# Kernel tuning notes

Measured on AMD Instinct MI355X. Metric: run time of the kernel, lower is better.

Reference implementation:

```python
import jax, jax.numpy as jnp
import numpy as np

B, T, DIM, HEADS, KV_HEADS = 2, 2048, 1024, 16, 4
HD = DIM // HEADS  # 64


def _rope(t, sin, cos):
    # interleaved RoPE: pairs (2i, 2i+1) rotated by the same angle
    rot = jnp.stack([-t[..., 1::2], t[..., ::2]], axis=-1).reshape(t.shape)
    return t * cos + rot * sin


def setup_inputs() -> dict:
    key = jax.random.key(0)
    kx, kq, kk, kv, ko = jax.random.split(key, 5)
    x = jax.random.normal(kx, (B, T, DIM), dtype=jnp.float32)
    # standard RoPE tables, [T, HD]
    pos = jnp.arange(T, dtype=jnp.float32)
    inv_freq = 1.0 / (10000.0 ** (jnp.arange(0, HD, 2, dtype=jnp.float32) / HD))
    ang = pos[:, None] * inv_freq[None, :]  # [T, HD/2]
    sin = jnp.repeat(jnp.sin(ang), 2, axis=-1)  # [T, HD]
    cos = jnp.repeat(jnp.cos(ang), 2, axis=-1)
    mask = jnp.ones((B, 1, T), dtype=jnp.float32)  # padding mask (all valid)
    s = 1.0 / np.sqrt(DIM).astype(np.float32)
    Wq = jax.random.normal(kq, (DIM, DIM), dtype=jnp.float32) * s
    Wk = jax.random.normal(kk, (DIM, KV_HEADS * HD), dtype=jnp.float32) * s
    Wv = jax.random.normal(kv, (DIM, KV_HEADS * HD), dtype=jnp.float32) * s
    Wo = jax.random.normal(ko, (DIM, DIM), dtype=jnp.float32) * s
    return {"x": x, "sin": sin, "cos": cos, "mask": mask,
            "Wq": Wq, "Wk": Wk, "Wv": Wv, "Wo": Wo}


def reference(x, sin, cos, mask, Wq, Wk, Wv, Wo):
    Bx, Tx, C = x.shape
    # projections -> [B, H, T, HD] / [B, KV, T, HD]
    q = (x @ Wq).reshape(Bx, Tx, HEADS, HD).transpose(0, 2, 1, 3)
    k = (x @ Wk).reshape(Bx, Tx, KV_HEADS, HD).transpose(0, 2, 1, 3)
    v = (x @ Wv).reshape(Bx, Tx, KV_HEADS, HD).transpose(0, 2, 1, 3)
    # RoPE (sin/cos [T, HD] broadcast over batch/heads)
    q = _rope(q, sin, cos)
    k = _rope(k, sin, cos)
    # GQA: expand kv heads to query heads
    groups = HEADS // KV_HEADS
    k = jnp.repeat(k, groups, axis=1)
    v = jnp.repeat(v, groups, axis=1)
    scores = jnp.einsum('bhqd,bhkd->bhqk', q, k) / np.sqrt(HD).astype(np.float32)
    causal = jnp.tril(jnp.ones((Tx, Tx), dtype=bool))  # [T, T]
    m = (mask[:, None, :, :] > 0) & causal  # [B,1,1,T] & [T,T] -> [B,1,T,T]
    scores = jnp.where(m, scores, jnp.asarray(-1e9, scores.dtype))
    attn = jax.nn.softmax(scores, axis=-1)
    out = jnp.einsum('bhqk,bhkd->bhqd', attn, v)
    out = out.transpose(0, 2, 1, 3).reshape(Bx, Tx, C)
    return out @ Wo
```

## Files before the change

### kernel.cpp

```cpp
#include <hip/hip_runtime.h>
#include <math.h>

typedef __attribute__((ext_vector_type(8))) short bf16x8;
typedef __attribute__((ext_vector_type(4))) float f32x4;
typedef __attribute__((ext_vector_type(4))) unsigned short u16x4;

#define B_    2
#define T_    2048
#define DIM_  1024
#define H_    16
#define KV_   4
#define HD_   64

#define QSCALE 0.1803368801111437f
#define SOFF  24.0f

static __device__ __forceinline__ unsigned short f2bf(float f) {
    union { float f; unsigned int u; } v; v.f = f;
    unsigned int r = v.u + 0x7fff + ((v.u >> 16) & 1);
    return (unsigned short)(r >> 16);
}

static __device__ __forceinline__ unsigned int pkbf(float lo, float hi) {
    union { float f; unsigned int u; } a, b; a.f = lo; b.f = hi;
    return ((a.u + 0x8000u) >> 16) | ((b.u + 0x8000u) & 0xffff0000u);
}

static __device__ __forceinline__ void gload16(const void* g, void* l) {
    __builtin_amdgcn_global_load_lds(
        (const __attribute__((address_space(1))) unsigned int*)g,
        (__attribute__((address_space(3))) unsigned int*)l, 16, 0, 0);
}

#define MFMA16(a, b, c) __builtin_amdgcn_mfma_f32_16x16x32_bf16(a, b, c, 0, 0, 0)

#define XB_OFF   0u
#define WT_OFF   4194304u
#define WOT_OFF  5767168u
#define QB_OFF   6815744u
#define KB_OFF   11010048u
#define VTB_OFF  12058624u
#define AB_OFF   13107200u
#define MB_OFF   17301504u

static __device__ __forceinline__ void wtrans_body(
    const float* __restrict__ W, unsigned short* __restrict__ Wt, int N,
    int n0, int k0, int tid, float (*Ts)[65])
{
    const int r = tid >> 4, c4 = (tid & 15) * 4;
    #pragma unroll
    for (int i = 0; i < 4; ++i) {
        float4 v = *(const float4*)&W[(size_t)(k0 + r + 16 * i) * N + n0 + c4];
        Ts[r + 16 * i][c4 + 0] = v.x; Ts[r + 16 * i][c4 + 1] = v.y;
        Ts[r + 16 * i][c4 + 2] = v.z; Ts[r + 16 * i][c4 + 3] = v.w;
    }
    __syncthreads();
    const int rn = tid >> 3, ck = (tid & 7) * 8;
    #pragma unroll
    for (int i = 0; i < 2; ++i) {
        int n = rn + 32 * i;
        unsigned short u[8];
        #pragma unroll
        for (int e = 0; e < 8; ++e) u[e] = f2bf(Ts[ck + e][n]);
        *(bf16x8*)&Wt[(size_t)(n0 + n) * 1024 + k0 + ck] = *(bf16x8*)u;
    }
}

__global__ __launch_bounds__(256) void prepass_kernel(
    const float* __restrict__ x,
    const float* __restrict__ Wq, const float* __restrict__ Wk,
    const float* __restrict__ Wv, const float* __restrict__ Wo,
    const float* __restrict__ maskp,
    unsigned short* __restrict__ xb, unsigned short* __restrict__ Wt,
    unsigned short* __restrict__ Wot, float* __restrict__ mbias)
{
    __shared__ float Ts[64][65];
    const int blk = blockIdx.x, tid = threadIdx.x;

    if (blk < 2048) {
        const size_t i = ((size_t)blk * 256 + tid) * 8;
        float4 a = *(const float4*)&x[i];
        float4 b = *(const float4*)&x[i + 4];
        unsigned short u[8] = {f2bf(a.x), f2bf(a.y), f2bf(a.z), f2bf(a.w),
                               f2bf(b.x), f2bf(b.y), f2bf(b.z), f2bf(b.w)};
        *(bf16x8*)&xb[i] = *(bf16x8*)u;
    } else if (blk < 2304) {
        const int sb = blk - 2048;
        wtrans_body(Wq, Wt, 1024, (sb & 15) * 64, (sb >> 4) * 64, tid, Ts);
    } else if (blk < 2368) {
        const int sb = blk - 2304;
        wtrans_body(Wk, Wt + 1024u * 1024u, 256, (sb & 3) * 64, (sb >> 2) * 64,
                    tid, Ts);
    } else if (blk < 2432) {
        const int sb = blk - 2368;
        wtrans_body(Wv, Wt + 1280u * 1024u, 256, (sb & 3) * 64, (sb >> 2) * 64,
                    tid, Ts);
    } else if (blk < 2688) {
        const int sb = blk - 2432;
        wtrans_body(Wo, Wot, 1024, (sb & 15) * 64, (sb >> 4) * 64, tid, Ts);
    } else {
        #pragma unroll
        for (int e = 0; e < 4; ++e) {
            const int i = tid * 16 + e * 4;
            f32x4 mv = *(const f32x4*)&maskp[i];
            f32x4 bv;
            #pragma unroll
            for (int j = 0; j < 4; ++j) bv[j] = mv[j] > 0.f ? -SOFF : -1e30f;
            *(f32x4*)&mbias[i] = bv;
        }
    }
}

__global__ __launch_bounds__(256) void qkv_mfma_kernel(
    const unsigned short* __restrict__ xb, const unsigned short* __restrict__ Wt,
    const float* __restrict__ sinp, const float* __restrict__ cosp,
    unsigned short* __restrict__ Qw, unsigned short* __restrict__ Kw,
    unsigned short* __restrict__ Vtw)
{
    __shared__ __align__(16) unsigned char As[8192];
    __shared__ __align__(16) unsigned char Bs[16384];

    const int tid = threadIdx.x, lane = tid & 63, w = tid >> 6;
    const int lr = lane & 15, lg = lane >> 4;
    const int wm = w >> 1, wn = w & 1;
    const int bn = blockIdx.x, bm = blockIdx.y;
    const int m0 = bm * 64, n0 = bn * 128;

    const int chunkR = lane >> 3;
    const int srcOff = 8 * ((lane & 7) ^ chunkR);

    f32x4 acc[2][4] = {};

    for (int k0 = 0; k0 < 1024; k0 += 64) {
        __syncthreads();
        #pragma unroll
        for (int i = 0; i < 6; ++i) {
            const int c = w * 6 + i;
            if (c < 8) {
                const int row = c * 8 + chunkR;
                gload16(xb + (size_t)(m0 + row) * 1024 + k0 + srcOff, As + c * 1024);
            } else {
                const int row = (c - 8) * 8 + chunkR;
                gload16(Wt + (size_t)(n0 + row) * 1024 + k0 + srcOff,
                        Bs + (c - 8) * 1024);
            }
        }
        __syncthreads();
        #pragma unroll
        for (int kk = 0; kk < 2; ++kk) {
            bf16x8 af[2], bfr[4];
            #pragma unroll
            for (int mf = 0; mf < 2; ++mf) {
                const int row = wm * 32 + mf * 16 + lr;
                af[mf] = *(const bf16x8*)(As + row * 128 +
                          ((kk * 64 + lg * 16) ^ ((row & 7) << 4)));
            }
            #pragma unroll
            for (int nf = 0; nf < 4; ++nf) {
                const int row = wn * 64 + nf * 16 + lr;
                bfr[nf] = *(const bf16x8*)(Bs + row * 128 +
                          ((kk * 64 + lg * 16) ^ ((row & 7) << 4)));
            }
            #pragma unroll
            for (int mf = 0; mf < 2; ++mf)
                #pragma unroll
                for (int nf = 0; nf < 4; ++nf)
                    acc[mf][nf] = MFMA16(af[mf], bfr[nf], acc[mf][nf]);
        }
    }

    const float rsign = (lane & 1) ? 1.f : -1.f;
    #pragma unroll
    for (int nf = 0; nf < 4; ++nf) {
        const int col = n0 + wn * 64 + nf * 16 + lr;
        #pragma unroll
        for (int mf = 0; mf < 2; ++mf) {
            const int mrow = m0 + wm * 32 + mf * 16 + lg * 4;
            const int b = mrow >> 11;
            const int t0 = mrow & 2047;
            if (col < 1280) {
                const int d = col & 63;
                #pragma unroll
                for (int r = 0; r < 4; ++r) {
                    float val = acc[mf][nf][r];
                    float partner = __shfl_xor(val, 1);
                    const int t = t0 + r;
                    float cs = cosp[t * 64 + d], sn = sinp[t * 64 + d];
                    float rv = val * cs + rsign * partner * sn;
                    if (col < 1024) {
                        const int h = col >> 6;
                        Qw[(((size_t)b * H_ + h) * T_ + t) * 64 + d] =
                            f2bf(rv * QSCALE);
                    } else {
                        const int kv = (col - 1024) >> 6;
                        char* krow = (char*)Kw +
                            ((((size_t)b * KV_ + kv) * T_ + t) << 7);
                        *(unsigned short*)(krow + ((2 * d) ^ ((t & 7) << 4))) =
                            f2bf(rv);
                    }
                }
            } else {
                const int cv = col - 1280, kv = cv >> 6, d = cv & 63;
                unsigned short u[4];
                #pragma unroll
                for (int r = 0; r < 4; ++r) u[r] = f2bf(acc[mf][nf][r]);
                char* vrow = (char*)Vtw +
                    ((((size_t)b * KV_ + kv) * 64 + d) * (size_t)T_ * 2);
                *(u16x4*)(vrow + ((2 * t0) ^ ((d & 7) << 4))) = *(u16x4*)u;
            }
        }
    }
}

__global__ __launch_bounds__(512, 4) void attn_kernel(
    const unsigned short* __restrict__ Qg, const unsigned short* __restrict__ Kg,
    const unsigned short* __restrict__ Vtg, const float* __restrict__ mbias,
    unsigned short* __restrict__ attn_out)
{
    __shared__ __align__(16) unsigned char Kl[2][8192];
    __shared__ __align__(16) unsigned char Vl[2][8192];
    __shared__ __align__(16) unsigned char Pl[16384];
    __shared__ float Lb[256];

    const int tid  = threadIdx.x;
    const int lane = tid & 63;
    const int w    = tid >> 6;
    const int grp  = w >> 2;
    const int wq   = w & 3;
    const int lr   = lane & 15;
    const int lg   = lane >> 4;

    const int bi   = blockIdx.x;
    const int qt   = 31 - (bi >> 5);
    const int bh   = bi & 31;
    const int h    = bh & 15;
    const int b    = bh >> 4;
    const int kvh  = h >> 2;
    const int q0   = qt * 64;
    const int qrow = q0 + wq * 16 + lr;

    const int nt    = qt + 1;
    const int mid   = nt >> 1;
    const int iters = nt - mid;

    const char* Kb = (const char*)(Kg  + ((size_t)b * KV_ + kvh) * T_ * HD_);
    const char* Vb = (const char*)(Vtg + ((size_t)b * KV_ + kvh) * HD_ * T_);
    const float* brow = mbias + b * T_;

    const int sr  = lane >> 3;
    const int scb = (lane & 7) * 16;
    unsigned char* Pw = &Pl[w * 2048];

    const unsigned short* Qbase =
        Qg + (((size_t)b * H_ + h) * T_ + qrow) * HD_;
    const bf16x8 qf0 = *(const bf16x8*)(Qbase + lg * 8);
    const bf16x8 qf1 = *(const bf16x8*)(Qbase + 32 + lg * 8);

    f32x4 o[4] = {};
    float l = 0.f;

    for (int it = 0; it < iters; ++it) {
        const int ktg = grp ? (mid + it) : it;
        const bool active = grp || (it < mid);
        const int k0 = ktg * 64;

        if (active) {
            #pragma unroll
            for (int i = 0; i < 2; ++i) {
                const int rb  = wq * 2 + i;
                const int row = rb * 8 + sr;
                gload16(Kb + (size_t)(k0 + row) * 128 + scb, &Kl[grp][rb * 1024]);
                gload16(Vb + (size_t)row * 4096 + 2 * k0 + scb, &Vl[grp][rb * 1024]);
            }
        }
        __syncthreads();

        if (active) {
            const unsigned char* Kc = Kl[grp];
            const unsigned char* Vc = Vl[grp];

            f32x4 bv[4];
            #pragma unroll
            for (int n = 0; n < 4; ++n)
                bv[n] = *(const f32x4*)&brow[k0 + 16 * n + 4 * lg];

            f32x4 s[4] = {};
            __builtin_amdgcn_s_setprio(1);
            #pragma unroll
            for (int n = 0; n < 4; ++n) {
                const int key = 16 * n + lr;
                #pragma unroll
                for (int ks = 0; ks < 2; ++ks) {
                    bf16x8 kb = *(const bf16x8*)(Kc +
                        ((key * 128 + 64 * ks + lg * 16) ^ ((key & 7) << 4)));
                    s[n] = MFMA16(kb, ks == 0 ? qf0 : qf1, s[n]);
                }
            }
            __builtin_amdgcn_s_setprio(0);

            if (ktg == qt) {
                #pragma unroll
                for (int n = 0; n < 4; ++n)
                    #pragma unroll
                    for (int r = 0; r < 4; ++r) {
                        const int keyg = k0 + 16 * n + 4 * lg + r;
                        s[n][r] = (keyg <= qrow) ? s[n][r] + bv[n][r] : -1e30f;
                    }
            } else {
                #pragma unroll
                for (int n = 0; n < 4; ++n)
                    #pragma unroll
                    for (int r = 0; r < 4; ++r) s[n][r] += bv[n][r];
            }
            #pragma unroll
            for (int n = 0; n < 4; ++n)
                #pragma unroll
                for (int r = 0; r < 4; ++r)
                    s[n][r] = exp2f(s[n][r]);

            float tsum[4];
            #pragma unroll
            for (int n = 0; n < 4; ++n)
                tsum[n] = (s[n][0] + s[n][1]) + (s[n][2] + s[n][3]);
            l += (tsum[0] + tsum[1]) + (tsum[2] + tsum[3]);

            #pragma unroll
            for (int n = 0; n < 4; ++n) {
                uint2 wv;
                wv.x = pkbf(s[n][0], s[n][1]);
                wv.y = pkbf(s[n][2], s[n][3]);
                *(uint2*)(Pw + ((lr * 128 + 32 * n + 8 * lg) ^ ((lr & 7) << 4))) = wv;
            }
            bf16x8 pa0 = *(const bf16x8*)(Pw + ((lr * 128 +      lg * 16) ^ ((lr & 7) << 4)));
            bf16x8 pa1 = *(const bf16x8*)(Pw + ((lr * 128 + 64 + lg * 16) ^ ((lr & 7) << 4)));

            __builtin_amdgcn_s_setprio(1);
            #pragma unroll
            for (int n = 0; n < 4; ++n) {
                const int d = 16 * n + lr;
                #pragma unroll
                for (int ks = 0; ks < 2; ++ks) {
                    bf16x8 vb = *(const bf16x8*)(Vc +
                        ((d * 128 + 64 * ks + lg * 16) ^ ((d & 7) << 4)));
                    o[n] = MFMA16(vb, ks == 0 ? pa0 : pa1, o[n]);
                }
            }
            __builtin_amdgcn_s_setprio(0);
        }

        __syncthreads();
    }

    const int slot = wq * 64 + lane;
    if (grp) {
        float* ob = (float*)Pl;
        #pragma unroll
        for (int n = 0; n < 4; ++n)
            *(f32x4*)&ob[slot * 16 + n * 4] = o[n];
        Lb[slot] = l;
    }
    __syncthreads();
    if (!grp) {
        const float* ob = (const float*)Pl;
        #pragma unroll
        for (int n = 0; n < 4; ++n) {
            f32x4 obv = *(const f32x4*)&ob[slot * 16 + n * 4];
            o[n] += obv;
        }
        float lf = l + Lb[slot];
        lf += __shfl_xor(lf, 16);
        lf += __shfl_xor(lf, 32);
        const float linv = 1.f / lf;
        unsigned short* orow =
            attn_out + ((size_t)b * T_ + qrow) * DIM_ + h * HD_;
        #pragma unroll
        for (int n = 0; n < 4; ++n) {
            unsigned short u[4];
            #pragma unroll
            for (int r = 0; r < 4; ++r) u[r] = f2bf(o[n][r] * linv);
            *(u16x4*)&orow[16 * n + 4 * lg] = *(u16x4*)u;
        }
    }
}

__global__ __launch_bounds__(256) void outproj_mfma_kernel(
    const unsigned short* __restrict__ Ab, const unsigned short* __restrict__ Wot,
    float* __restrict__ out)
{
    __shared__ __align__(16) unsigned char As[8192];
    __shared__ __align__(16) unsigned char Bs[16384];

    const int tid = threadIdx.x, lane = tid & 63, w = tid >> 6;
    const int lr = lane & 15, lg = lane >> 4;
    const int wm = w >> 1, wn = w & 1;
    const int bn = blockIdx.x, bm = blockIdx.y;
    const int m0 = bm * 64, n0 = bn * 128;

    const int chunkR = lane >> 3;
    const int srcOff = 8 * ((lane & 7) ^ chunkR);

    f32x4 acc[2][4] = {};

    for (int k0 = 0; k0 < 1024; k0 += 64) {
        __syncthreads();
        #pragma unroll
        for (int i = 0; i < 6; ++i) {
            const int c = w * 6 + i;
            if (c < 8) {
                const int row = c * 8 + chunkR;
                gload16(Ab + (size_t)(m0 + row) * 1024 + k0 + srcOff, As + c * 1024);
            } else {
                const int row = (c - 8) * 8 + chunkR;
                gload16(Wot + (size_t)(n0 + row) * 1024 + k0 + srcOff,
                        Bs + (c - 8) * 1024);
            }
        }
        __syncthreads();
        #pragma unroll
        for (int kk = 0; kk < 2; ++kk) {
            bf16x8 af[2], bfr[4];
            #pragma unroll
            for (int mf = 0; mf < 2; ++mf) {
                const int row = wm * 32 + mf * 16 + lr;
                af[mf] = *(const bf16x8*)(As + row * 128 +
                          ((kk * 64 + lg * 16) ^ ((row & 7) << 4)));
            }
            #pragma unroll
            for (int nf = 0; nf < 4; ++nf) {
                const int row = wn * 64 + nf * 16 + lr;
                bfr[nf] = *(const bf16x8*)(Bs + row * 128 +
                          ((kk * 64 + lg * 16) ^ ((row & 7) << 4)));
            }
            #pragma unroll
            for (int mf = 0; mf < 2; ++mf)
                #pragma unroll
                for (int nf = 0; nf < 4; ++nf)
                    acc[mf][nf] = MFMA16(af[mf], bfr[nf], acc[mf][nf]);
        }
    }

    #pragma unroll
    for (int nf = 0; nf < 4; ++nf) {
        const int col = n0 + wn * 64 + nf * 16 + lr;
        #pragma unroll
        for (int mf = 0; mf < 2; ++mf) {
            const int mrow = m0 + wm * 32 + mf * 16 + lg * 4;
            #pragma unroll
            for (int r = 0; r < 4; ++r)
                out[(size_t)(mrow + r) * 1024 + col] = acc[mf][nf][r];
        }
    }
}

extern "C" void kernel_launch(void* const* d_in, const int* in_sizes, int n_in,
                              void* d_out, int out_size, void* d_ws, size_t ws_size,
                              hipStream_t stream)
{
    const float* x     = (const float*)d_in[0];
    const float* sinp  = (const float*)d_in[1];
    const float* cosp  = (const float*)d_in[2];
    const float* maskp = (const float*)d_in[3];
    const float* Wq    = (const float*)d_in[4];
    const float* Wk    = (const float*)d_in[5];
    const float* Wv    = (const float*)d_in[6];
    const float* Wo    = (const float*)d_in[7];

    unsigned short* wsb = (unsigned short*)d_ws;
    unsigned short* xb  = wsb + XB_OFF;
    unsigned short* Wt  = wsb + WT_OFF;
    unsigned short* Wot = wsb + WOT_OFF;
    unsigned short* Qw  = wsb + QB_OFF;
    unsigned short* Kw  = wsb + KB_OFF;
    unsigned short* Vtw = wsb + VTB_OFF;
    unsigned short* Ab  = wsb + AB_OFF;
    float* mbias        = (float*)(wsb + MB_OFF);
    float* out = (float*)d_out;

    prepass_kernel<<<2689, 256, 0, stream>>>(x, Wq, Wk, Wv, Wo, maskp,
                                             xb, Wt, Wot, mbias);
    qkv_mfma_kernel<<<dim3(12, 64), 256, 0, stream>>>(xb, Wt, sinp, cosp,
                                                      Qw, Kw, Vtw);
    attn_kernel<<<dim3(1024), 512, 0, stream>>>(
        Qw, Kw, Vtw, mbias, Ab);
    outproj_mfma_kernel<<<dim3(8, 64), 256, 0, stream>>>(Ab, Wot, out);
}
```

Measured before the change: 103.9 us.

## Share GQA K/V tiles across four query heads with double-buffered loads

The attention kernel now gives each block the four query heads that share one KV head, each with 32 query rows. Every K/V tile loaded into LDS is therefore reused by all four heads instead of being fetched once per head. The old intra-block split of the key range across two wave groups, and its LDS reduction at the end, is replaced by a single sequential pass with a double-buffered prefetch of the next K/V tile. The grid is halved, which reduces global K/V traffic and removes the merge step, at the cost of longer per-block serial loops and less parallelism along the causal key range.

```diff
diff --git a/kernel.cpp b/kernel.cpp
--- a/kernel.cpp
+++ b/kernel.cpp
@@ -219,167 +219,138 @@
 {
     __shared__ __align__(16) unsigned char Kl[2][8192];
     __shared__ __align__(16) unsigned char Vl[2][8192];
-    __shared__ __align__(16) unsigned char Pl[16384];
-    __shared__ float Lb[256];
+    __shared__ __align__(16) unsigned char Pl[8][2048];
 
     const int tid  = threadIdx.x;
     const int lane = tid & 63;
     const int w    = tid >> 6;
-    const int grp  = w >> 2;
-    const int wq   = w & 3;
+    const int hidx = w >> 1;
+    const int wq   = w & 1;
     const int lr   = lane & 15;
     const int lg   = lane >> 4;
 
-    const int bi   = blockIdx.x;
-    const int qt   = 31 - (bi >> 5);
-    const int bh   = bi & 31;
-    const int h    = bh & 15;
-    const int b    = bh >> 4;
-    const int kvh  = h >> 2;
-    const int q0   = qt * 64;
+    const int bi  = blockIdx.x;
+    const int bh2 = bi & 7;
+    const int g32 = 63 - (bi >> 3);
+    const int b   = bh2 >> 2;
+    const int kvh = bh2 & 3;
+    const int h   = kvh * 4 + hidx;
+    const int q0  = g32 * 32;
     const int qrow = q0 + wq * 16 + lr;
-
-    const int nt    = qt + 1;
-    const int mid   = nt >> 1;
-    const int iters = nt - mid;
+    const int nt   = ((q0 + 31) >> 6) + 1;
 
     const char* Kb = (const char*)(Kg  + ((size_t)b * KV_ + kvh) * T_ * HD_);
     const char* Vb = (const char*)(Vtg + ((size_t)b * KV_ + kvh) * HD_ * T_);
     const float* brow = mbias + b * T_;
 
-    const int sr  = lane >> 3;
-    const int scb = (lane & 7) * 16;
-    unsigned char* Pw = &Pl[w * 2048];
-
-    const unsigned short* Qbase =
-        Qg + (((size_t)b * H_ + h) * T_ + qrow) * HD_;
+    const int srow = w * 8 + (lane >> 3);
+    const int scb  = (lane & 7) * 16;
+    unsigned char* Pw = &Pl[w][0];
+
+    const unsigned short* Qbase = Qg + (((size_t)b * H_ + h) * T_ + qrow) * HD_;
     const bf16x8 qf0 = *(const bf16x8*)(Qbase + lg * 8);
     const bf16x8 qf1 = *(const bf16x8*)(Qbase + 32 + lg * 8);
 
     f32x4 o[4] = {};
     float l = 0.f;
 
-    for (int it = 0; it < iters; ++it) {
-        const int ktg = grp ? (mid + it) : it;
-        const bool active = grp || (it < mid);
-        const int k0 = ktg * 64;
-
-        if (active) {
-            #pragma unroll
-            for (int i = 0; i < 2; ++i) {
-                const int rb  = wq * 2 + i;
-                const int row = rb * 8 + sr;
-                gload16(Kb + (size_t)(k0 + row) * 128 + scb, &Kl[grp][rb * 1024]);
-                gload16(Vb + (size_t)row * 4096 + 2 * k0 + scb, &Vl[grp][rb * 1024]);
-            }
-        }
+    gload16(Kb + (size_t)srow * 128 + scb, &Kl[0][(size_t)srow * 128 + scb]);
+    gload16(Vb + (size_t)srow * 4096 + scb, &Vl[0][(size_t)srow * 128 + scb]);
+
+    for (int t = 0; t < nt; ++t) {
+        const int k0 = t * 64;
         __syncthreads();
 
-        if (active) {
-            const unsigned char* Kc = Kl[grp];
-            const unsigned char* Vc = Vl[grp];
-
-            f32x4 bv[4];
+        if (t + 1 < nt) {
+            const int k0n = k0 + 64;
+            unsigned char* Kn = &Kl[(t + 1) & 1][(size_t)srow * 128 + scb];
+            unsigned char* Vn = &Vl[(t + 1) & 1][(size_t)srow * 128 + scb];
+            gload16(Kb + (size_t)(k0n + srow) * 128 + scb, Kn);
+            gload16(Vb + (size_t)srow * 4096 + 2 * k0n + scb, Vn);
+        }
+
+        const unsigned char* Kc = Kl[t & 1];
+        const unsigned char* Vc = Vl[t & 1];
+
+        f32x4 bv[4];
+        #pragma unroll
+        for (int n = 0; n < 4; ++n)
+            bv[n] = *(const f32x4*)&brow[k0 + 16 * n + 4 * lg];
+
+        f32x4 s[4] = {};
+        __builtin_amdgcn_s_setprio(1);
+        #pragma unroll
+        for (int n = 0; n < 4; ++n) {
+            const int key = 16 * n + lr;
+            #pragma unroll
+            for (int ks = 0; ks < 2; ++ks) {
+                bf16x8 kb = *(const bf16x8*)(Kc +
+                    ((key * 128 + 64 * ks + lg * 16) ^ ((key & 7) << 4)));
+                s[n] = MFMA16(kb, ks == 0 ? qf0 : qf1, s[n]);
+            }
+        }
+        __builtin_amdgcn_s_setprio(0);
+
+        if (t == nt - 1) {
             #pragma unroll
             for (int n = 0; n < 4; ++n)
-                bv[n] = *(const f32x4*)&brow[k0 + 16 * n + 4 * lg];
-
-            f32x4 s[4] = {};
-            __builtin_amdgcn_s_setprio(1);
-            #pragma unroll
-            for (int n = 0; n < 4; ++n) {
-                const int key = 16 * n + lr;
-                #pragma unroll
-                for (int ks = 0; ks < 2; ++ks) {
-                    bf16x8 kb = *(const bf16x8*)(Kc +
-                        ((key * 128 + 64 * ks + lg * 16) ^ ((key & 7) << 4)));
-                    s[n] = MFMA16(kb, ks == 0 ? qf0 : qf1, s[n]);
+                #pragma unroll
+                for (int r = 0; r < 4; ++r) {
+                    const int keyg = k0 + 16 * n + 4 * lg + r;
+                    s[n][r] = (keyg <= qrow) ? s[n][r] + bv[n][r] : -1e30f;
                 }
-            }
-            __builtin_amdgcn_s_setprio(0);
-
-            if (ktg == qt) {
-                #pragma unroll
-                for (int n = 0; n < 4; ++n)
-                    #pragma unroll
-                    for (int r = 0; r < 4; ++r) {
-                        const int keyg = k0 + 16 * n + 4 * lg + r;
-                        s[n][r] = (keyg <= qrow) ? s[n][r] + bv[n][r] : -1e30f;
-                    }
-            } else {
-                #pragma unroll
-                for (int n = 0; n < 4; ++n)
-                    #pragma unroll
-                    for (int r = 0; r < 4; ++r) s[n][r] += bv[n][r];
-            }
+        } else {
             #pragma unroll
             for (int n = 0; n < 4; ++n)
                 #pragma unroll
-                for (int r = 0; r < 4; ++r)
-                    s[n][r] = exp2f(s[n][r]);
-
-            float tsum[4];
-            #pragma unroll
-            for (int n = 0; n < 4; ++n)
-                tsum[n] = (s[n][0] + s[n][1]) + (s[n][2] + s[n][3]);
-            l += (tsum[0] + tsum[1]) + (tsum[2] + tsum[3]);
-
-            #pragma unroll
-            for (int n = 0; n < 4; ++n) {
-                uint2 wv;
-                wv.x = pkbf(s[n][0], s[n][1]);
-                wv.y = pkbf(s[n][2], s[n][3]);
-                *(uint2*)(Pw + ((lr * 128 + 32 * n + 8 * lg) ^ ((lr & 7) << 4))) = wv;
-            }
-            bf16x8 pa0 = *(const bf16x8*)(Pw + ((lr * 128 +      lg * 16) ^ ((lr & 7) << 4)));
-            bf16x8 pa1 = *(const bf16x8*)(Pw + ((lr * 128 + 64 + lg * 16) ^ ((lr & 7) << 4)));
-
-            __builtin_amdgcn_s_setprio(1);
-            #pragma unroll
-            for (int n = 0; n < 4; ++n) {
-                const int d = 16 * n + lr;
-                #pragma unroll
-                for (int ks = 0; ks < 2; ++ks) {
-                    bf16x8 vb = *(const bf16x8*)(Vc +
-                        ((d * 128 + 64 * ks + lg * 16) ^ ((d & 7) << 4)));
-                    o[n] = MFMA16(vb, ks == 0 ? pa0 : pa1, o[n]);
-                }
-            }
-            __builtin_amdgcn_s_setprio(0);
-        }
-
-        __syncthreads();
-    }
-
-    const int slot = wq * 64 + lane;
-    if (grp) {
-        float* ob = (float*)Pl;
+                for (int r = 0; r < 4; ++r) s[n][r] += bv[n][r];
+        }
         #pragma unroll
         for (int n = 0; n < 4; ++n)
-            *(f32x4*)&ob[slot * 16 + n * 4] = o[n];
-        Lb[slot] = l;
-    }
-    __syncthreads();
-    if (!grp) {
-        const float* ob = (const float*)Pl;
+            #pragma unroll
+            for (int r = 0; r < 4; ++r)
+                s[n][r] = exp2f(s[n][r]);
+
+        float tsum[4];
+        #pragma unroll
+        for (int n = 0; n < 4; ++n)
+            tsum[n] = (s[n][0] + s[n][1]) + (s[n][2] + s[n][3]);
+        l += (tsum[0] + tsum[1]) + (tsum[2] + tsum[3]);
+
         #pragma unroll
         for (int n = 0; n < 4; ++n) {
-            f32x4 obv = *(const f32x4*)&ob[slot * 16 + n * 4];
-            o[n] += obv;
-        }
-        float lf = l + Lb[slot];
-        lf += __shfl_xor(lf, 16);
-        lf += __shfl_xor(lf, 32);
-        const float linv = 1.f / lf;
-        unsigned short* orow =
-            attn_out + ((size_t)b * T_ + qrow) * DIM_ + h * HD_;
+            uint2 wv;
+            wv.x = pkbf(s[n][0], s[n][1]);
+            wv.y = pkbf(s[n][2], s[n][3]);
+            *(uint2*)(Pw + ((lr * 128 + 32 * n + 8 * lg) ^ ((lr & 7) << 4))) = wv;
+        }
+        bf16x8 pa0 = *(const bf16x8*)(Pw + ((lr * 128 +      lg * 16) ^ ((lr & 7) << 4)));
+        bf16x8 pa1 = *(const bf16x8*)(Pw + ((lr * 128 + 64 + lg * 16) ^ ((lr & 7) << 4)));
+
+        __builtin_amdgcn_s_setprio(1);
         #pragma unroll
         for (int n = 0; n < 4; ++n) {
-            unsigned short u[4];
-            #pragma unroll
-            for (int r = 0; r < 4; ++r) u[r] = f2bf(o[n][r] * linv);
-            *(u16x4*)&orow[16 * n + 4 * lg] = *(u16x4*)u;
-        }
+            const int d = 16 * n + lr;
+            #pragma unroll
+            for (int ks = 0; ks < 2; ++ks) {
+                bf16x8 vb = *(const bf16x8*)(Vc +
+                    ((d * 128 + 64 * ks + lg * 16) ^ ((d & 7) << 4)));
+                o[n] = MFMA16(vb, ks == 0 ? pa0 : pa1, o[n]);
+            }
+        }
+        __builtin_amdgcn_s_setprio(0);
+    }
+
+    l += __shfl_xor(l, 16);
+    l += __shfl_xor(l, 32);
+    const float linv = 1.f / l;
+    unsigned short* orow = attn_out + ((size_t)b * T_ + qrow) * DIM_ + h * HD_;
+    #pragma unroll
+    for (int n = 0; n < 4; ++n) {
+        unsigned short u[4];
+        #pragma unroll
+        for (int r = 0; r < 4; ++r) u[r] = f2bf(o[n][r] * linv);
+        *(u16x4*)&orow[16 * n + 4 * lg] = *(u16x4*)u;
     }
 }
 
@@ -480,7 +451,7 @@
                                              xb, Wt, Wot, mbias);
     qkv_mfma_kernel<<<dim3(12, 64), 256, 0, stream>>>(xb, Wt, sinp, cosp,
                                                       Qw, Kw, Vtw);
-    attn_kernel<<<dim3(1024), 512, 0, stream>>>(
+    attn_kernel<<<dim3(512), 512, 0, stream>>>(
         Qw, Kw, Vtw, mbias, Ab);
     outproj_mfma_kernel<<<dim3(8, 64), 256, 0, stream>>>(Ab, Wot, out);
 }
```

After: 112.8 us. 8.6% more time.

## Use 32-key tiles with double-buffered LDS and balanced split across wave groups

Applied to the files above, without the earlier changes.

Shrinks the attention key tile from 64 to 32 keys and double-buffers K/V in LDS, so the next tile's global loads are issued before the current tile is computed and one barrier per iteration is dropped. The two wave groups now each take exactly half of the 32-key tiles, removing the idle iterations the first group had under the old 64-key split. The V swizzle changes to match 64-byte rows, and the P scratch is padded to an 80-byte row stride. The cost is twice as many iterations, each with less MFMA work, plus the same per-iteration barrier overhead.

```diff
diff --git a/kernel.cpp b/kernel.cpp
--- a/kernel.cpp
+++ b/kernel.cpp
@@ -206,7 +206,7 @@
                 for (int r = 0; r < 4; ++r) u[r] = f2bf(acc[mf][nf][r]);
                 char* vrow = (char*)Vtw +
                     ((((size_t)b * KV_ + kv) * 64 + d) * (size_t)T_ * 2);
-                *(u16x4*)(vrow + ((2 * t0) ^ ((d & 7) << 4))) = *(u16x4*)u;
+                *(u16x4*)(vrow + ((2 * t0) ^ ((d & 3) << 4))) = *(u16x4*)u;
             }
         }
     }
@@ -217,9 +217,9 @@
     const unsigned short* __restrict__ Vtg, const float* __restrict__ mbias,
     unsigned short* __restrict__ attn_out)
 {
-    __shared__ __align__(16) unsigned char Kl[2][8192];
-    __shared__ __align__(16) unsigned char Vl[2][8192];
-    __shared__ __align__(16) unsigned char Pl[16384];
+    __shared__ __align__(16) unsigned char Kl[2][2][4096];
+    __shared__ __align__(16) unsigned char Vl[2][2][4096];
+    __shared__ __align__(16) unsigned char Pl[8][1280];
     __shared__ float Lb[256];
 
     const int tid  = threadIdx.x;
@@ -239,121 +239,115 @@
     const int q0   = qt * 64;
     const int qrow = q0 + wq * 16 + lr;
 
-    const int nt    = qt + 1;
-    const int mid   = nt >> 1;
-    const int iters = nt - mid;
+    const int nt     = 2 * qt + 2;
+    const int iters  = qt + 1;
+    const int ktbase = grp ? (qt + 1) : 0;
 
     const char* Kb = (const char*)(Kg  + ((size_t)b * KV_ + kvh) * T_ * HD_);
     const char* Vb = (const char*)(Vtg + ((size_t)b * KV_ + kvh) * HD_ * T_);
     const float* brow = mbias + b * T_;
 
-    const int sr  = lane >> 3;
-    const int scb = (lane & 7) * 16;
-    unsigned char* Pw = &Pl[w * 2048];
-
-    const unsigned short* Qbase =
-        Qg + (((size_t)b * H_ + h) * T_ + qrow) * HD_;
+    const int krow = wq * 8 + (lane >> 3);
+    const int kcb  = (lane & 7) * 16;
+    const int vrow = wq * 16 + (lane >> 2);
+    const int vcb  = (lane & 3) * 16;
+    const int dstoff = wq * 1024 + lane * 16;
+    unsigned char* Pw = &Pl[w][0];
+
+    const unsigned short* Qbase = Qg + (((size_t)b * H_ + h) * T_ + qrow) * HD_;
     const bf16x8 qf0 = *(const bf16x8*)(Qbase + lg * 8);
     const bf16x8 qf1 = *(const bf16x8*)(Qbase + 32 + lg * 8);
 
     f32x4 o[4] = {};
     float l = 0.f;
 
+    {
+        const int k0p = ktbase * 32;
+        gload16(Kb + (size_t)(k0p + krow) * 128 + kcb, &Kl[grp][0][dstoff]);
+        gload16(Vb + (size_t)vrow * 4096 + 2 * k0p + vcb, &Vl[grp][0][dstoff]);
+    }
+
     for (int it = 0; it < iters; ++it) {
-        const int ktg = grp ? (mid + it) : it;
-        const bool active = grp || (it < mid);
-        const int k0 = ktg * 64;
-
-        if (active) {
-            #pragma unroll
-            for (int i = 0; i < 2; ++i) {
-                const int rb  = wq * 2 + i;
-                const int row = rb * 8 + sr;
-                gload16(Kb + (size_t)(k0 + row) * 128 + scb, &Kl[grp][rb * 1024]);
-                gload16(Vb + (size_t)row * 4096 + 2 * k0 + scb, &Vl[grp][rb * 1024]);
-            }
-        }
+        const int ktg = ktbase + it;
+        const int k0  = ktg * 32;
         __syncthreads();
 
-        if (active) {
-            const unsigned char* Kc = Kl[grp];
-            const unsigned char* Vc = Vl[grp];
-
-            f32x4 bv[4];
-            #pragma unroll
-            for (int n = 0; n < 4; ++n)
-                bv[n] = *(const f32x4*)&brow[k0 + 16 * n + 4 * lg];
-
-            f32x4 s[4] = {};
-            __builtin_amdgcn_s_setprio(1);
-            #pragma unroll
-            for (int n = 0; n < 4; ++n) {
-                const int key = 16 * n + lr;
-                #pragma unroll
-                for (int ks = 0; ks < 2; ++ks) {
-                    bf16x8 kb = *(const bf16x8*)(Kc +
-                        ((key * 128 + 64 * ks + lg * 16) ^ ((key & 7) << 4)));
-                    s[n] = MFMA16(kb, ks == 0 ? qf0 : qf1, s[n]);
-                }
-            }
-            __builtin_amdgcn_s_setprio(0);
-
-            if (ktg == qt) {
-                #pragma unroll
-                for (int n = 0; n < 4; ++n)
-                    #pragma unroll
-                    for (int r = 0; r < 4; ++r) {
-                        const int keyg = k0 + 16 * n + 4 * lg + r;
-                        s[n][r] = (keyg <= qrow) ? s[n][r] + bv[n][r] : -1e30f;
-                    }
-            } else {
-                #pragma unroll
-                for (int n = 0; n < 4; ++n)
-                    #pragma unroll
-                    for (int r = 0; r < 4; ++r) s[n][r] += bv[n][r];
-            }
-            #pragma unroll
-            for (int n = 0; n < 4; ++n)
-                #pragma unroll
-                for (int r = 0; r < 4; ++r)
-                    s[n][r] = exp2f(s[n][r]);
-
-            float tsum[4];
-            #pragma unroll
-            for (int n = 0; n < 4; ++n)
-                tsum[n] = (s[n][0] + s[n][1]) + (s[n][2] + s[n][3]);
-            l += (tsum[0] + tsum[1]) + (tsum[2] + tsum[3]);
-
-            #pragma unroll
-            for (int n = 0; n < 4; ++n) {
-                uint2 wv;
-                wv.x = pkbf(s[n][0], s[n][1]);
-                wv.y = pkbf(s[n][2], s[n][3]);
-                *(uint2*)(Pw + ((lr * 128 + 32 * n + 8 * lg) ^ ((lr & 7) << 4))) = wv;
-            }
-            bf16x8 pa0 = *(const bf16x8*)(Pw + ((lr * 128 +      lg * 16) ^ ((lr & 7) << 4)));
-            bf16x8 pa1 = *(const bf16x8*)(Pw + ((lr * 128 + 64 + lg * 16) ^ ((lr & 7) << 4)));
-
-            __builtin_amdgcn_s_setprio(1);
-            #pragma unroll
-            for (int n = 0; n < 4; ++n) {
-                const int d = 16 * n + lr;
-                #pragma unroll
-                for (int ks = 0; ks < 2; ++ks) {
-                    bf16x8 vb = *(const bf16x8*)(Vc +
-                        ((d * 128 + 64 * ks + lg * 16) ^ ((d & 7) << 4)));
-                    o[n] = MFMA16(vb, ks == 0 ? pa0 : pa1, o[n]);
-                }
-            }
-            __builtin_amdgcn_s_setprio(0);
-        }
-
-        __syncthreads();
-    }
-
+        if (it + 1 < iters) {
+            const int k0n = k0 + 32;
+            gload16(Kb + (size_t)(k0n + krow) * 128 + kcb,
+                    &Kl[grp][(it + 1) & 1][dstoff]);
+            gload16(Vb + (size_t)vrow * 4096 + 2 * k0n + vcb,
+                    &Vl[grp][(it + 1) & 1][dstoff]);
+        }
+
+        const unsigned char* Kc = Kl[grp][it & 1];
+        const unsigned char* Vc = Vl[grp][it & 1];
+
+        f32x4 bv0 = *(const f32x4*)&brow[k0 + 4 * lg];
+        f32x4 bv1 = *(const f32x4*)&brow[k0 + 16 + 4 * lg];
+
+        f32x4 s0 = {}, s1 = {};
+        __builtin_amdgcn_s_setprio(1);
+        {
+            const int r0 = lr, r1 = 16 + lr;
+            const int swz = (lr & 7) << 4;
+            bf16x8 kb;
+            kb = *(const bf16x8*)(Kc + r0 * 128 + ((16 * lg)      ^ swz));
+            s0 = MFMA16(kb, qf0, s0);
+            kb = *(const bf16x8*)(Kc + r0 * 128 + ((64 + 16 * lg) ^ swz));
+            s0 = MFMA16(kb, qf1, s0);
+            kb = *(const bf16x8*)(Kc + r1 * 128 + ((16 * lg)      ^ swz));
+            s1 = MFMA16(kb, qf0, s1);
+            kb = *(const bf16x8*)(Kc + r1 * 128 + ((64 + 16 * lg) ^ swz));
+            s1 = MFMA16(kb, qf1, s1);
+        }
+        __builtin_amdgcn_s_setprio(0);
+
+        if (ktg >= nt - 2) {
+            #pragma unroll
+            for (int r = 0; r < 4; ++r) {
+                const int kg0 = k0 + 4 * lg + r;
+                const int kg1 = kg0 + 16;
+                s0[r] = (kg0 <= qrow) ? s0[r] + bv0[r] : -1e30f;
+                s1[r] = (kg1 <= qrow) ? s1[r] + bv1[r] : -1e30f;
+            }
+        } else {
+            #pragma unroll
+            for (int r = 0; r < 4; ++r) {
+                s0[r] += bv0[r];
+                s1[r] += bv1[r];
+            }
+        }
+        #pragma unroll
+        for (int r = 0; r < 4; ++r) {
+            s0[r] = exp2f(s0[r]);
+            s1[r] = exp2f(s1[r]);
+        }
+        l += ((s0[0] + s0[1]) + (s0[2] + s0[3])) +
+             ((s1[0] + s1[1]) + (s1[2] + s1[3]));
+
+        uint2 w0, w1;
+        w0.x = pkbf(s0[0], s0[1]); w0.y = pkbf(s0[2], s0[3]);
+        w1.x = pkbf(s1[0], s1[1]); w1.y = pkbf(s1[2], s1[3]);
+        *(uint2*)(Pw + lr * 80 + 8 * lg)      = w0;
+        *(uint2*)(Pw + lr * 80 + 32 + 8 * lg) = w1;
+        bf16x8 pa = *(const bf16x8*)(Pw + lr * 80 + 16 * lg);
+
+        __builtin_amdgcn_s_setprio(1);
+        #pragma unroll
+        for (int n = 0; n < 4; ++n) {
+            const int row = 16 * n + lr;
+            bf16x8 vb = *(const bf16x8*)(Vc + row * 64 +
+                         ((16 * lg) ^ ((row & 3) << 4)));
+            o[n] = MFMA16(vb, pa, o[n]);
+        }
+        __builtin_amdgcn_s_setprio(0);
+    }
+
+    __syncthreads();
     const int slot = wq * 64 + lane;
     if (grp) {
-        float* ob = (float*)Pl;
+        float* ob = (float*)Kl;
         #pragma unroll
         for (int n = 0; n < 4; ++n)
             *(f32x4*)&ob[slot * 16 + n * 4] = o[n];
@@ -361,7 +355,7 @@
     }
     __syncthreads();
     if (!grp) {
-        const float* ob = (const float*)Pl;
+        const float* ob = (const float*)Kl;
         #pragma unroll
         for (int n = 0; n < 4; ++n) {
             f32x4 obv = *(const f32x4*)&ob[slot * 16 + n * 4];
```

New measurement: 105.0 us. Within noise of the previous version (+1.1%).

## Restructure attention to 32x32 MFMA tiles with 128-row query blocks and double-buffered KV

Applied to the files above, without the earlier changes.

The attention kernel now uses 32x32x16 bf16 MFMA instead of 16x16x32. Each block covers 128 query rows with 32-key tiles, and the causal work is split evenly between the two wave groups. K/V tiles are double-buffered in LDS, so the next tile's loads overlap compute and one barrier per iteration is removed. The V-transpose swizzle in the QKV kernel changes to match the new layout. The grid is halved, which risks lower occupancy and load imbalance in exchange for more reuse per block and fewer barriers.

```diff
diff --git a/kernel.cpp b/kernel.cpp
--- a/kernel.cpp
+++ b/kernel.cpp
@@ -3,6 +3,7 @@
 
 typedef __attribute__((ext_vector_type(8))) short bf16x8;
 typedef __attribute__((ext_vector_type(4))) float f32x4;
+typedef __attribute__((ext_vector_type(16))) float f32x16;
 typedef __attribute__((ext_vector_type(4))) unsigned short u16x4;
 
 #define B_    2
@@ -33,6 +34,7 @@
 }
 
 #define MFMA16(a, b, c) __builtin_amdgcn_mfma_f32_16x16x32_bf16(a, b, c, 0, 0, 0)
+#define MFMA32(a, b, c) __builtin_amdgcn_mfma_f32_32x32x16_bf16(a, b, c, 0, 0, 0)
 
 #define XB_OFF   0u
 #define WT_OFF   4194304u
@@ -206,7 +208,7 @@
                 for (int r = 0; r < 4; ++r) u[r] = f2bf(acc[mf][nf][r]);
                 char* vrow = (char*)Vtw +
                     ((((size_t)b * KV_ + kv) * 64 + d) * (size_t)T_ * 2);
-                *(u16x4*)(vrow + ((2 * t0) ^ ((d & 7) << 4))) = *(u16x4*)u;
+                *(u16x4*)(vrow + ((2 * t0) ^ ((d & 3) << 4))) = *(u16x4*)u;
             }
         }
     }
@@ -217,169 +219,184 @@
     const unsigned short* __restrict__ Vtg, const float* __restrict__ mbias,
     unsigned short* __restrict__ attn_out)
 {
-    __shared__ __align__(16) unsigned char Kl[2][8192];
-    __shared__ __align__(16) unsigned char Vl[2][8192];
-    __shared__ __align__(16) unsigned char Pl[16384];
-    __shared__ float Lb[256];
+    __shared__ __align__(16) unsigned char lds[50176];
+    unsigned char* KL = lds;
+    unsigned char* VL = lds + 16384;
+    float* LB = (float*)(lds + 49152);
 
     const int tid  = threadIdx.x;
     const int lane = tid & 63;
     const int w    = tid >> 6;
     const int grp  = w >> 2;
     const int wq   = w & 3;
-    const int lr   = lane & 15;
-    const int lg   = lane >> 4;
+    const int l31  = lane & 31;
+    const int lhi  = lane >> 5;
 
     const int bi   = blockIdx.x;
-    const int qt   = 31 - (bi >> 5);
+    const int qg   = 15 - (bi >> 5);
     const int bh   = bi & 31;
     const int h    = bh & 15;
     const int b    = bh >> 4;
     const int kvh  = h >> 2;
-    const int q0   = qt * 64;
-    const int qrow = q0 + wq * 16 + lr;
-
-    const int nt    = qt + 1;
-    const int mid   = nt >> 1;
-    const int iters = nt - mid;
+    const int q0w  = qg * 128 + wq * 32;
+    const int qrow = q0w + l31;
+
+    const int iters  = 2 * qg + 2;
+    const int ktbase = grp ? iters : 0;
 
     const char* Kb = (const char*)(Kg  + ((size_t)b * KV_ + kvh) * T_ * HD_);
     const char* Vb = (const char*)(Vtg + ((size_t)b * KV_ + kvh) * HD_ * T_);
     const float* brow = mbias + b * T_;
 
-    const int sr  = lane >> 3;
-    const int scb = (lane & 7) * 16;
-    unsigned char* Pw = &Pl[w * 2048];
-
-    const unsigned short* Qbase =
-        Qg + (((size_t)b * H_ + h) * T_ + qrow) * HD_;
-    const bf16x8 qf0 = *(const bf16x8*)(Qbase + lg * 8);
-    const bf16x8 qf1 = *(const bf16x8*)(Qbase + 32 + lg * 8);
-
-    f32x4 o[4] = {};
+    const int krow = wq * 8 + (lane >> 3);
+    const int kcb  = (lane & 7) * 16;
+    const int vrow = wq * 16 + (lane >> 2);
+    const int vcb  = (lane & 3) * 16;
+    const int dstoff = wq * 1024 + lane * 16;
+    unsigned char* Pw = lds + 32768 + w * 2048;
+    const int pswz = (l31 & 3) << 4;
+
+    const unsigned short* Qbase = Qg + (((size_t)b * H_ + h) * T_ + qrow) * HD_;
+    bf16x8 qf[4];
+    #pragma unroll
+    for (int st = 0; st < 4; ++st)
+        qf[st] = *(const bf16x8*)(Qbase + 16 * st + 8 * lhi);
+
+    f32x16 o[2] = {};
     float l = 0.f;
 
+    {
+        const int k0p = ktbase * 32;
+        gload16(Kb + (size_t)(k0p + krow) * 128 + kcb, KL + grp * 8192 + dstoff);
+        gload16(Vb + (size_t)vrow * 4096 + 2 * k0p + vcb, VL + grp * 8192 + dstoff);
+    }
+
     for (int it = 0; it < iters; ++it) {
-        const int ktg = grp ? (mid + it) : it;
-        const bool active = grp || (it < mid);
-        const int k0 = ktg * 64;
-
-        if (active) {
-            #pragma unroll
-            for (int i = 0; i < 2; ++i) {
-                const int rb  = wq * 2 + i;
-                const int row = rb * 8 + sr;
-                gload16(Kb + (size_t)(k0 + row) * 128 + scb, &Kl[grp][rb * 1024]);
-                gload16(Vb + (size_t)row * 4096 + 2 * k0 + scb, &Vl[grp][rb * 1024]);
-            }
-        }
+        const int k0 = (ktbase + it) * 32;
         __syncthreads();
 
-        if (active) {
-            const unsigned char* Kc = Kl[grp];
-            const unsigned char* Vc = Vl[grp];
-
-            f32x4 bv[4];
-            #pragma unroll
-            for (int n = 0; n < 4; ++n)
-                bv[n] = *(const f32x4*)&brow[k0 + 16 * n + 4 * lg];
-
-            f32x4 s[4] = {};
-            __builtin_amdgcn_s_setprio(1);
-            #pragma unroll
-            for (int n = 0; n < 4; ++n) {
-                const int key = 16 * n + lr;
-                #pragma unroll
-                for (int ks = 0; ks < 2; ++ks) {
-                    bf16x8 kb = *(const bf16x8*)(Kc +
-                        ((key * 128 + 64 * ks + lg * 16) ^ ((key & 7) << 4)));
-                    s[n] = MFMA16(kb, ks == 0 ? qf0 : qf1, s[n]);
+        if (it + 1 < iters) {
+            const int k0n = k0 + 32;
+            const int boff = grp * 8192 + ((it + 1) & 1) * 4096 + dstoff;
+            gload16(Kb + (size_t)(k0n + krow) * 128 + kcb, KL + boff);
+            gload16(Vb + (size_t)vrow * 4096 + 2 * k0n + vcb, VL + boff);
+        }
+
+        const unsigned char* Kc = KL + grp * 8192 + (it & 1) * 4096;
+        const unsigned char* Vc = VL + grp * 8192 + (it & 1) * 4096;
+
+        f32x4 bv[4];
+        #pragma unroll
+        for (int g = 0; g < 4; ++g)
+            bv[g] = *(const f32x4*)&brow[k0 + 8 * g + 4 * lhi];
+
+        f32x16 s = {};
+        __builtin_amdgcn_s_setprio(1);
+        {
+            const int swzk = (l31 & 7) << 4;
+            #pragma unroll
+            for (int st = 0; st < 4; ++st) {
+                bf16x8 kb = *(const bf16x8*)(Kc + l31 * 128 +
+                             ((32 * st + 16 * lhi) ^ swzk));
+                s = MFMA32(kb, qf[st], s);
+            }
+        }
+        __builtin_amdgcn_s_setprio(0);
+
+        if (k0 + 31 > q0w) {
+            #pragma unroll
+            for (int g = 0; g < 4; ++g)
+                #pragma unroll
+                for (int r = 0; r < 4; ++r) {
+                    const int keyg = k0 + 8 * g + 4 * lhi + r;
+                    s[4 * g + r] = (keyg <= qrow) ? s[4 * g + r] + bv[g][r]
+                                                  : -1e30f;
                 }
-            }
-            __builtin_amdgcn_s_setprio(0);
-
-            if (ktg == qt) {
-                #pragma unroll
-                for (int n = 0; n < 4; ++n)
-                    #pragma unroll
-                    for (int r = 0; r < 4; ++r) {
-                        const int keyg = k0 + 16 * n + 4 * lg + r;
-                        s[n][r] = (keyg <= qrow) ? s[n][r] + bv[n][r] : -1e30f;
-                    }
-            } else {
-                #pragma unroll
-                for (int n = 0; n < 4; ++n)
-                    #pragma unroll
-                    for (int r = 0; r < 4; ++r) s[n][r] += bv[n][r];
-            }
-            #pragma unroll
-            for (int n = 0; n < 4; ++n)
+        } else {
+            #pragma unroll
+            for (int g = 0; g < 4; ++g)
                 #pragma unroll
                 for (int r = 0; r < 4; ++r)
-                    s[n][r] = exp2f(s[n][r]);
-
-            float tsum[4];
-            #pragma unroll
-            for (int n = 0; n < 4; ++n)
-                tsum[n] = (s[n][0] + s[n][1]) + (s[n][2] + s[n][3]);
-            l += (tsum[0] + tsum[1]) + (tsum[2] + tsum[3]);
-
-            #pragma unroll
-            for (int n = 0; n < 4; ++n) {
-                uint2 wv;
-                wv.x = pkbf(s[n][0], s[n][1]);
-                wv.y = pkbf(s[n][2], s[n][3]);
-                *(uint2*)(Pw + ((lr * 128 + 32 * n + 8 * lg) ^ ((lr & 7) << 4))) = wv;
-            }
-            bf16x8 pa0 = *(const bf16x8*)(Pw + ((lr * 128 +      lg * 16) ^ ((lr & 7) << 4)));
-            bf16x8 pa1 = *(const bf16x8*)(Pw + ((lr * 128 + 64 + lg * 16) ^ ((lr & 7) << 4)));
-
-            __builtin_amdgcn_s_setprio(1);
-            #pragma unroll
-            for (int n = 0; n < 4; ++n) {
-                const int d = 16 * n + lr;
-                #pragma unroll
-                for (int ks = 0; ks < 2; ++ks) {
-                    bf16x8 vb = *(const bf16x8*)(Vc +
-                        ((d * 128 + 64 * ks + lg * 16) ^ ((d & 7) << 4)));
-                    o[n] = MFMA16(vb, ks == 0 ? pa0 : pa1, o[n]);
-                }
-            }
-            __builtin_amdgcn_s_setprio(0);
-        }
-
-        __syncthreads();
-    }
-
+                    s[4 * g + r] += bv[g][r];
+        }
+        #pragma unroll
+        for (int i = 0; i < 16; ++i) s[i] = exp2f(s[i]);
+
+        float ts[4];
+        #pragma unroll
+        for (int g = 0; g < 4; ++g)
+            ts[g] = (s[4 * g] + s[4 * g + 1]) + (s[4 * g + 2] + s[4 * g + 3]);
+        l += (ts[0] + ts[1]) + (ts[2] + ts[3]);
+
+        #pragma unroll
+        for (int g = 0; g < 4; ++g) {
+            uint2 wv;
+            wv.x = pkbf(s[4 * g], s[4 * g + 1]);
+            wv.y = pkbf(s[4 * g + 2], s[4 * g + 3]);
+            *(uint2*)(Pw + l31 * 64 + ((16 * g + 8 * lhi) ^ pswz)) = wv;
+        }
+        bf16x8 pb0 = *(const bf16x8*)(Pw + l31 * 64 + ((16 * lhi) ^ pswz));
+        bf16x8 pb1 = *(const bf16x8*)(Pw + l31 * 64 + ((32 + 16 * lhi) ^ pswz));
+
+        __builtin_amdgcn_s_setprio(1);
+        #pragma unroll
+        for (int ks = 0; ks < 2; ++ks) {
+            const bf16x8 pb = ks ? pb1 : pb0;
+            #pragma unroll
+            for (int db = 0; db < 2; ++db) {
+                const int row = db * 32 + l31;
+                bf16x8 vb = *(const bf16x8*)(Vc + row * 64 +
+                             ((32 * ks + 16 * lhi) ^ ((l31 & 3) << 4)));
+                o[db] = MFMA32(vb, pb, o[db]);
+            }
+        }
+        __builtin_amdgcn_s_setprio(0);
+    }
+
+    __syncthreads();
     const int slot = wq * 64 + lane;
     if (grp) {
-        float* ob = (float*)Pl;
-        #pragma unroll
-        for (int n = 0; n < 4; ++n)
-            *(f32x4*)&ob[slot * 16 + n * 4] = o[n];
-        Lb[slot] = l;
+        #pragma unroll
+        for (int db = 0; db < 2; ++db)
+            #pragma unroll
+            for (int g = 0; g < 4; ++g) {
+                f32x4 v4 = { o[db][4 * g], o[db][4 * g + 1],
+                             o[db][4 * g + 2], o[db][4 * g + 3] };
+                const int c = db * 4 + g;
+                *(f32x4*)(lds + slot * 128 + ((c * 16) ^ ((slot & 7) << 4))) = v4;
+            }
+        LB[slot] = l;
     }
     __syncthreads();
     if (!grp) {
-        const float* ob = (const float*)Pl;
-        #pragma unroll
-        for (int n = 0; n < 4; ++n) {
-            f32x4 obv = *(const f32x4*)&ob[slot * 16 + n * 4];
-            o[n] += obv;
-        }
-        float lf = l + Lb[slot];
-        lf += __shfl_xor(lf, 16);
+        #pragma unroll
+        for (int db = 0; db < 2; ++db)
+            #pragma unroll
+            for (int g = 0; g < 4; ++g) {
+                const int c = db * 4 + g;
+                f32x4 v4 = *(const f32x4*)(lds + slot * 128 +
+                                           ((c * 16) ^ ((slot & 7) << 4)));
+                o[db][4 * g]     += v4[0];
+                o[db][4 * g + 1] += v4[1];
+                o[db][4 * g + 2] += v4[2];
+                o[db][4 * g + 3] += v4[3];
+            }
+        float lf = l + LB[slot];
         lf += __shfl_xor(lf, 32);
         const float linv = 1.f / lf;
         unsigned short* orow =
             attn_out + ((size_t)b * T_ + qrow) * DIM_ + h * HD_;
         #pragma unroll
-        for (int n = 0; n < 4; ++n) {
-            unsigned short u[4];
-            #pragma unroll
-            for (int r = 0; r < 4; ++r) u[r] = f2bf(o[n][r] * linv);
-            *(u16x4*)&orow[16 * n + 4 * lg] = *(u16x4*)u;
-        }
+        for (int db = 0; db < 2; ++db)
+            #pragma unroll
+            for (int g = 0; g < 4; ++g) {
+                const int d = db * 32 + 8 * g + 4 * lhi;
+                unsigned short u[4];
+                #pragma unroll
+                for (int r = 0; r < 4; ++r)
+                    u[r] = f2bf(o[db][4 * g + r] * linv);
+                *(u16x4*)&orow[d] = *(u16x4*)u;
+            }
     }
 }
 
@@ -480,7 +497,7 @@
                                              xb, Wt, Wot, mbias);
     qkv_mfma_kernel<<<dim3(12, 64), 256, 0, stream>>>(xb, Wt, sinp, cosp,
                                                       Qw, Kw, Vtw);
-    attn_kernel<<<dim3(1024), 512, 0, stream>>>(
+    attn_kernel<<<dim3(512), 512, 0, stream>>>(
         Qw, Kw, Vtw, mbias, Ab);
     outproj_mfma_kernel<<<dim3(8, 64), 256, 0, stream>>>(Ab, Wot, out);
 }
```

Result: slower. 121.9 us (+17.3%).
